# Performance work log

Measured on AMD Instinct MI355X. Metric: run time of the kernel, lower is better.

The kernel has to match this reference:

```python
import jax, jax.numpy as jnp
import numpy as np

EPS = 1e-12
TAU = 1.0

def _normalize(x, axis=-1):
    # matches torch.nn.functional.normalize (p=2, eps=1e-12)
    n = jnp.linalg.norm(x, axis=axis, keepdims=True)
    return x / jnp.maximum(n, EPS)

def setup_inputs() -> dict:
    key = jax.random.key(0)
    ks = jax.random.split(key, 6)
    N, B, D, K = 8192, 512, 64, 4
    input_rating = jax.random.uniform(ks[0], (B, N), dtype=jnp.float32)
    # row-normalized-scale adjacency (mimics a normalized item-item graph)
    item_adj = jax.random.uniform(ks[1], (N, N), dtype=jnp.float32) * (2.0 / N)
    item_emb = jax.random.normal(ks[2], (N, D), dtype=jnp.float32) * float(np.sqrt(2.0 / (N + D)))
    proto_emb = jax.random.normal(ks[3], (K, D), dtype=jnp.float32) * float(np.sqrt(2.0 / (K + D)))
    enc_w = jax.random.normal(ks[4], (2 * D, N), dtype=jnp.float32) * float(np.sqrt(2.0 / (N + 2 * D)))
    enc_b = jax.random.normal(ks[5], (2 * D,), dtype=jnp.float32) * 0.01
    return {"input_rating": input_rating, "item_adj": item_adj, "item_emb": item_emb,
            "proto_emb": proto_emb, "enc_w": enc_w, "enc_b": enc_b}

def reference(input_rating, item_adj, item_emb, proto_emb, enc_w, enc_b):
    D = enc_b.shape[0] // 2
    prototypes = _normalize(proto_emb)          # [K, D]
    items = _normalize(item_emb)                # [N, D]
    cates = jax.nn.softmax(items @ prototypes.T / TAU, axis=-1)  # [N, K] (eval: mode branch)
    # per-prototype masked ratings, vectorized over K: [K, B, N]
    x_k = input_rating[None, :, :] * cates.T[:, None, :]
    x_k = _normalize(x_k)                       # fn.normalize(x_k, p=2) over items dim
    # two-hop propagation through dense item-item adjacency
    tmp = jnp.einsum('kbn,nm->kbm', x_k, item_adj)
    tmp = jnp.einsum('kbn,nm->kbm', tmp, item_adj)
    x = (tmp + x_k) / 2.0                       # dropout is identity in eval
    h = jnp.einsum('kbn,on->kbo', x, enc_w) + enc_b  # [K, B, 2D]
    mu = _normalize(h[..., :D])                 # [K, B, D]
    logvar = -h[..., D:]                        # [K, B, D]
    z = _normalize(mu)                          # eval: reparameterize returns mu
    logits_k = jnp.einsum('kbd,nd->kbn', z, items) / TAU
    probs = jnp.sum(jnp.exp(logits_k) * cates.T[:, None, :], axis=0)  # [B, N]
    logits = jnp.log(probs)
    return logits, mu, logvar
```

## Files before the change

kernel.cpp:

```cpp
#include <hip/hip_runtime.h>

typedef __attribute__((ext_vector_type(8))) short short8;
typedef __attribute__((ext_vector_type(4))) float f32x4;

#define AS3P(x) ((__attribute__((address_space(3))) void*)(x))
#define AS1P(x) ((const __attribute__((address_space(1))) void*)(x))

__device__ __forceinline__ unsigned short f2bf(float f) {
    unsigned int u = __float_as_uint(f);
    u += 0x7fffu + ((u >> 16) & 1u);
    return (unsigned short)(u >> 16);
}
__device__ __forceinline__ float bf2f(unsigned short b) {
    return __uint_as_float(((unsigned int)b) << 16);
}
__device__ __forceinline__ unsigned int pk2bf(float a, float b) {
    return (unsigned int)f2bf(a) | ((unsigned int)f2bf(b) << 16);
}
__device__ __forceinline__ float waveReduceSum(float v) {
    #pragma unroll
    for (int off = 32; off; off >>= 1) v += __shfl_xor(v, off, 64);
    return v;
}

__global__ __launch_bounds__(256) void k_mega(const float* __restrict__ adj,
                                              unsigned short* __restrict__ adj_bf,
                                              const float* __restrict__ enc_w,
                                              unsigned short* __restrict__ encw,
                                              const float* __restrict__ item_emb,
                                              const float* __restrict__ proto,
                                              unsigned short* __restrict__ items_bf,
                                              float* __restrict__ catesT) {
    __shared__ float sp[256];
    int bx = blockIdx.x, tid = threadIdx.x;
    if (bx < 32768) {
        size_t i = ((size_t)bx * 256 + tid) * 8;
        f32x4 a = __builtin_nontemporal_load((const f32x4*)(adj + i));
        f32x4 b = __builtin_nontemporal_load((const f32x4*)(adj + i + 4));
        uint4 pk;
        pk.x = pk2bf(a[0], a[1]); pk.y = pk2bf(a[2], a[3]);
        pk.z = pk2bf(b[0], b[1]); pk.w = pk2bf(b[2], b[3]);
        *(uint4*)(adj_bf + i) = pk;
        return;
    }
    if (bx < 33280) {
        size_t i = (((size_t)bx - 32768) * 256 + tid) * 8;
        float4 a = *(const float4*)(enc_w + i);
        float4 b = *(const float4*)(enc_w + i + 4);
        uint4 pk;
        pk.x = pk2bf(a.x, a.y); pk.y = pk2bf(a.z, a.w);
        pk.z = pk2bf(b.x, b.y); pk.w = pk2bf(b.z, b.w);
        *(uint4*)(encw + i) = pk;
        return;
    }
    sp[tid] = proto[tid];
    __syncthreads();
    {
        float v = sp[tid];
        float ss = waveReduceSum(v * v);
        sp[tid] = v * (1.f / fmaxf(sqrtf(ss), 1e-12f));
    }
    __syncthreads();
    int i = (bx - 33280) * 256 + tid;
    const float4* row = (const float4*)(item_emb + (size_t)i * 64);
    float4 f[16];
    float ss = 0.f;
    #pragma unroll
    for (int q = 0; q < 16; ++q) {
        f[q] = row[q];
        ss += f[q].x * f[q].x + f[q].y * f[q].y + f[q].z * f[q].z + f[q].w * f[q].w;
    }
    float inv = 1.f / fmaxf(sqrtf(ss), 1e-12f);
    float dots[4] = {0.f, 0.f, 0.f, 0.f};
    unsigned short* ob = items_bf + (size_t)i * 64;
    #pragma unroll
    for (int q = 0; q < 16; ++q) {
        f[q].x *= inv; f[q].y *= inv; f[q].z *= inv; f[q].w *= inv;
        #pragma unroll
        for (int k = 0; k < 4; ++k) {
            dots[k] += f[q].x * sp[k * 64 + q * 4 + 0] + f[q].y * sp[k * 64 + q * 4 + 1]
                     + f[q].z * sp[k * 64 + q * 4 + 2] + f[q].w * sp[k * 64 + q * 4 + 3];
        }
    }
    #pragma unroll
    for (int q = 0; q < 16; q += 2) {
        uint4 pk;
        pk.x = pk2bf(f[q].x, f[q].y);         pk.y = pk2bf(f[q].z, f[q].w);
        pk.z = pk2bf(f[q + 1].x, f[q + 1].y); pk.w = pk2bf(f[q + 1].z, f[q + 1].w);
        *(uint4*)(ob + q * 4) = pk;
    }
    float m = fmaxf(fmaxf(dots[0], dots[1]), fmaxf(dots[2], dots[3]));
    float e0 = expf(dots[0] - m), e1 = expf(dots[1] - m), e2 = expf(dots[2] - m), e3 = expf(dots[3] - m);
    float is = 1.f / (e0 + e1 + e2 + e3);
    catesT[0 * 8192 + i] = e0 * is;
    catesT[1 * 8192 + i] = e1 * is;
    catesT[2 * 8192 + i] = e2 * is;
    catesT[3 * 8192 + i] = e3 * is;
}

__global__ __launch_bounds__(256) void k_gemm_part(const unsigned short* __restrict__ A,
                                                   const unsigned short* __restrict__ B,
                                                   unsigned short* __restrict__ Cout,
                                                   int M, int ksplit, int lda, int ldb, int ldc) {
    __shared__ unsigned short lA[128 * 64];
    __shared__ unsigned short lB[128 * 64];
    int tid = threadIdx.x;
    int lane = tid & 63;
    int w = tid >> 6;
    int wr = w >> 1, wc = w & 1;
    int mBase = blockIdx.y * 128;
    int nBase = blockIdx.x * 128;
    int Kbeg = blockIdx.z * ksplit;
    int Kend = Kbeg + ksplit;

    f32x4 acc[4][4] = {};

    const unsigned short* Ablk = A + (size_t)mBase * lda;
    const unsigned short* Bblk = B + (size_t)nBase * ldb;
    int srow = tid >> 3;
    int scg = (tid & 7) ^ (srow & 7);
    char* ldsA_w = (char*)lA + w * 1024;
    char* ldsB_w = (char*)lB + w * 1024;

    for (int k0 = Kbeg; k0 < Kend; k0 += 64) {
        __syncthreads();
        #pragma unroll
        for (int it = 0; it < 4; ++it) {
            const unsigned short* ga = Ablk + (size_t)(it * 32 + srow) * lda + k0 + scg * 8;
            __builtin_amdgcn_global_load_lds(AS1P(ga), AS3P(ldsA_w + it * 4096), 16, 0, 0);
            const unsigned short* gb = Bblk + (size_t)(it * 32 + srow) * ldb + k0 + scg * 8;
            __builtin_amdgcn_global_load_lds(AS1P(gb), AS3P(ldsB_w + it * 4096), 16, 0, 0);
        }
        __syncthreads();
        #pragma unroll
        for (int kk = 0; kk < 2; ++kk) {
            short8 af[4], bfr[4];
            #pragma unroll
            for (int i = 0; i < 4; ++i) {
                int rowa = wr * 64 + i * 16 + (lane & 15);
                int slot = kk * 4 + (lane >> 4);
                af[i] = *(const short8*)((const char*)lA + rowa * 128 + ((slot ^ (rowa & 7)) * 16));
                int rowb = wc * 64 + i * 16 + (lane & 15);
                bfr[i] = *(const short8*)((const char*)lB + rowb * 128 + ((slot ^ (rowb & 7)) * 16));
            }
            #pragma unroll
            for (int i = 0; i < 4; ++i)
                #pragma unroll
                for (int j = 0; j < 4; ++j)
                    acc[i][j] = __builtin_amdgcn_mfma_f32_16x16x32_bf16(af[i], bfr[j], acc[i][j], 0, 0, 0);
        }
    }

    unsigned short* outP = Cout + (size_t)blockIdx.z * M * ldc;
    #pragma unroll
    for (int i = 0; i < 4; ++i) {
        int rbase = mBase + wr * 64 + i * 16 + (lane >> 4) * 4;
        #pragma unroll
        for (int j = 0; j < 4; ++j) {
            int col = nBase + wc * 64 + j * 16 + (lane & 15);
            #pragma unroll
            for (int r = 0; r < 4; ++r)
                outP[(size_t)(rbase + r) * ldc + col] = f2bf(acc[i][j][r]);
        }
    }
}

__global__ __launch_bounds__(256) void k_redW(const unsigned short* __restrict__ part,
                                              unsigned short* __restrict__ W1T,
                                              const float* __restrict__ rating,
                                              const float* __restrict__ catesT,
                                              unsigned short* __restrict__ rating_bf,
                                              float* __restrict__ inv4) {
    int tid = threadIdx.x;
    if (blockIdx.x < 512) {
        size_t base = ((size_t)blockIdx.x * 256 + tid) * 8;
        float a[8] = {0.f,0.f,0.f,0.f,0.f,0.f,0.f,0.f};
        #pragma unroll
        for (int sp = 0; sp < 8; ++sp) {
            uint4 v = *(const uint4*)(part + (size_t)sp * 1048576 + base);
            a[0] += bf2f((unsigned short)(v.x & 0xffff)); a[1] += bf2f((unsigned short)(v.x >> 16));
            a[2] += bf2f((unsigned short)(v.y & 0xffff)); a[3] += bf2f((unsigned short)(v.y >> 16));
            a[4] += bf2f((unsigned short)(v.z & 0xffff)); a[5] += bf2f((unsigned short)(v.z >> 16));
            a[6] += bf2f((unsigned short)(v.w & 0xffff)); a[7] += bf2f((unsigned short)(v.w >> 16));
        }
        uint4 pk;
        pk.x = pk2bf(a[0], a[1]); pk.y = pk2bf(a[2], a[3]);
        pk.z = pk2bf(a[4], a[5]); pk.w = pk2bf(a[6], a[7]);
        *(uint4*)(W1T + base) = pk;
        return;
    }
    __shared__ float t[16];
    int b = blockIdx.x - 512;
    const float* row = rating + (size_t)b * 8192;
    float s0 = 0.f, s1 = 0.f, s2 = 0.f, s3 = 0.f;
    #pragma unroll
    for (int j = 0; j < 8; ++j) {
        int i4 = tid + j * 256;
        f32x4 r = __builtin_nontemporal_load((const f32x4*)(row + i4 * 4));
        ushort4 pk;
        pk.x = f2bf(r[0]); pk.y = f2bf(r[1]); pk.z = f2bf(r[2]); pk.w = f2bf(r[3]);
        *(ushort4*)(rating_bf + (size_t)b * 8192 + i4 * 4) = pk;
        float4 c0 = *(const float4*)(catesT + 0 * 8192 + i4 * 4);
        float4 c1 = *(const float4*)(catesT + 1 * 8192 + i4 * 4);
        float4 c2 = *(const float4*)(catesT + 2 * 8192 + i4 * 4);
        float4 c3 = *(const float4*)(catesT + 3 * 8192 + i4 * 4);
        float px, py, pz, pw;
        px = r[0] * c0.x; py = r[1] * c0.y; pz = r[2] * c0.z; pw = r[3] * c0.w;
        s0 += px * px + py * py + pz * pz + pw * pw;
        px = r[0] * c1.x; py = r[1] * c1.y; pz = r[2] * c1.z; pw = r[3] * c1.w;
        s1 += px * px + py * py + pz * pz + pw * pw;
        px = r[0] * c2.x; py = r[1] * c2.y; pz = r[2] * c2.z; pw = r[3] * c2.w;
        s2 += px * px + py * py + pz * pz + pw * pw;
        px = r[0] * c3.x; py = r[1] * c3.y; pz = r[2] * c3.z; pw = r[3] * c3.w;
        s3 += px * px + py * py + pz * pz + pw * pw;
    }
    s0 = waveReduceSum(s0); s1 = waveReduceSum(s1);
    s2 = waveReduceSum(s2); s3 = waveReduceSum(s3);
    if ((tid & 63) == 0) {
        int w = tid >> 6;
        t[w * 4 + 0] = s0; t[w * 4 + 1] = s1; t[w * 4 + 2] = s2; t[w * 4 + 3] = s3;
    }
    __syncthreads();
    if (tid < 4) {
        float ss = t[0 * 4 + tid] + t[1 * 4 + tid] + t[2 * 4 + tid] + t[3 * 4 + tid];
        inv4[b * 4 + tid] = 1.f / fmaxf(sqrtf(ss), 1e-12f);
    }
}

__global__ __launch_bounds__(256) void k_red_G(const unsigned short* __restrict__ part,
                                               const float* __restrict__ enc_w,
                                               const float* __restrict__ catesT,
                                               unsigned short* __restrict__ G) {
    size_t base = ((size_t)blockIdx.x * 256 + threadIdx.x) * 8;
    int o = (int)(base >> 13);
    int n = (int)(base & 8191);
    float a[8] = {0.f,0.f,0.f,0.f,0.f,0.f,0.f,0.f};
    #pragma unroll
    for (int sp = 0; sp < 8; ++sp) {
        uint4 v = *(const uint4*)(part + (size_t)sp * 1048576 + base);
        a[0] += bf2f((unsigned short)(v.x & 0xffff)); a[1] += bf2f((unsigned short)(v.x >> 16));
        a[2] += bf2f((unsigned short)(v.y & 0xffff)); a[3] += bf2f((unsigned short)(v.y >> 16));
        a[4] += bf2f((unsigned short)(v.z & 0xffff)); a[5] += bf2f((unsigned short)(v.z >> 16));
        a[6] += bf2f((unsigned short)(v.w & 0xffff)); a[7] += bf2f((unsigned short)(v.w >> 16));
    }
    float4 e0 = *(const float4*)(enc_w + base);
    float4 e1 = *(const float4*)(enc_w + base + 4);
    a[0] = 0.5f * (a[0] + e0.x); a[1] = 0.5f * (a[1] + e0.y);
    a[2] = 0.5f * (a[2] + e0.z); a[3] = 0.5f * (a[3] + e0.w);
    a[4] = 0.5f * (a[4] + e1.x); a[5] = 0.5f * (a[5] + e1.y);
    a[6] = 0.5f * (a[6] + e1.z); a[7] = 0.5f * (a[7] + e1.w);
    #pragma unroll
    for (int k = 0; k < 4; ++k) {
        float4 c0 = *(const float4*)(catesT + (size_t)k * 8192 + n);
        float4 c1 = *(const float4*)(catesT + (size_t)k * 8192 + n + 4);
        uint4 pk;
        pk.x = pk2bf(a[0] * c0.x, a[1] * c0.y); pk.y = pk2bf(a[2] * c0.z, a[3] * c0.w);
        pk.z = pk2bf(a[4] * c1.x, a[5] * c1.y); pk.w = pk2bf(a[6] * c1.z, a[7] * c1.w);
        *(uint4*)(G + (size_t)(k * 128 + o) * 8192 + n) = pk;
    }
}

__global__ __launch_bounds__(128) void k_reduce_h2(const unsigned short* __restrict__ hpart,
                                                   const float* __restrict__ enc_b,
                                                   const float* __restrict__ inv4,
                                                   unsigned short* __restrict__ mu_bf,
                                                   float* __restrict__ outp) {
    int r = blockIdx.x;
    int k = r >> 9, b = r & 511;
    int o = threadIdx.x;
    float s = 0.f;
    #pragma unroll
    for (int sp = 0; sp < 32; ++sp)
        s += bf2f(hpart[(size_t)sp * 262144 + (size_t)b * 512 + k * 128 + o]);
    s = s * inv4[b * 4 + k] + enc_b[o];
    const size_t MU0 = (size_t)512 * 8192;
    const size_t LV0 = MU0 + (size_t)2048 * 64;
    if (o < 64) {
        float ss = s * s;
        #pragma unroll
        for (int off = 32; off; off >>= 1) ss += __shfl_xor(ss, off, 64);
        float inv = 1.f / fmaxf(sqrtf(ss), 1e-12f);
        float mv = s * inv;
        outp[MU0 + (size_t)r * 64 + o] = mv;
        mu_bf[(size_t)r * 64 + o] = f2bf(mv);
    } else {
        outp[LV0 + (size_t)r * 64 + (o - 64)] = -s;
    }
}

__global__ __launch_bounds__(256) void k_logits_mfma(const unsigned short* __restrict__ mu_bf,
                                                     const unsigned short* __restrict__ items_bf,
                                                     const float* __restrict__ catesT,
                                                     float* __restrict__ out) {
    __shared__ unsigned short lA[128 * 64];
    __shared__ unsigned short lB[128 * 64];
    int tid = threadIdx.x;
    int lane = tid & 63, w = tid >> 6, wr = w >> 1, wc = w & 1;
    int nBase = blockIdx.x * 128, bBase = blockIdx.y * 128;
    int srow = tid >> 3;
    int scg = (tid & 7) ^ (srow & 7);
    char* ldsA_w = (char*)lA + w * 1024;
    char* ldsB_w = (char*)lB + w * 1024;

    #pragma unroll
    for (int it = 0; it < 4; ++it) {
        const unsigned short* gb = items_bf + (size_t)(nBase + it * 32 + srow) * 64 + scg * 8;
        __builtin_amdgcn_global_load_lds(AS1P(gb), AS3P(ldsB_w + it * 4096), 16, 0, 0);
    }

    f32x4 p[4][4] = {};
    for (int k = 0; k < 4; ++k) {
        __syncthreads();
        #pragma unroll
        for (int it = 0; it < 4; ++it) {
            const unsigned short* ga = mu_bf + (size_t)(k * 512 + bBase + it * 32 + srow) * 64 + scg * 8;
            __builtin_amdgcn_global_load_lds(AS1P(ga), AS3P(ldsA_w + it * 4096), 16, 0, 0);
        }
        __syncthreads();
        f32x4 acc[4][4] = {};
        #pragma unroll
        for (int kk = 0; kk < 2; ++kk) {
            short8 af[4], bfr[4];
            #pragma unroll
            for (int i = 0; i < 4; ++i) {
                int rowa = wr * 64 + i * 16 + (lane & 15);
                int slot = kk * 4 + (lane >> 4);
                af[i] = *(const short8*)((const char*)lA + rowa * 128 + ((slot ^ (rowa & 7)) * 16));
                int rowb = wc * 64 + i * 16 + (lane & 15);
                bfr[i] = *(const short8*)((const char*)lB + rowb * 128 + ((slot ^ (rowb & 7)) * 16));
            }
            #pragma unroll
            for (int i = 0; i < 4; ++i)
                #pragma unroll
                for (int j = 0; j < 4; ++j)
                    acc[i][j] = __builtin_amdgcn_mfma_f32_16x16x32_bf16(af[i], bfr[j], acc[i][j], 0, 0, 0);
        }
        #pragma unroll
        for (int j = 0; j < 4; ++j) {
            int col = nBase + wc * 64 + j * 16 + (lane & 15);
            float c = catesT[(size_t)k * 8192 + col];
            #pragma unroll
            for (int i = 0; i < 4; ++i)
                #pragma unroll
                for (int r = 0; r < 4; ++r)
                    p[i][j][r] += __expf(acc[i][j][r]) * c;
        }
    }
    #pragma unroll
    for (int i = 0; i < 4; ++i) {
        int rbase = bBase + wr * 64 + i * 16 + (lane >> 4) * 4;
        #pragma unroll
        for (int j = 0; j < 4; ++j) {
            int col = nBase + wc * 64 + j * 16 + (lane & 15);
            #pragma unroll
            for (int r = 0; r < 4; ++r)
                out[(size_t)(rbase + r) * 8192 + col] = __logf(p[i][j][r]);
        }
    }
}

extern "C" void kernel_launch(void* const* d_in, const int* in_sizes, int n_in,
                              void* d_out, int out_size, void* d_ws, size_t ws_size,
                              hipStream_t stream) {
    const float* rating   = (const float*)d_in[0];
    const float* adj      = (const float*)d_in[1];
    const float* item_emb = (const float*)d_in[2];
    const float* proto    = (const float*)d_in[3];
    const float* enc_w    = (const float*)d_in[4];
    const float* enc_b    = (const float*)d_in[5];
    float* out = (float*)d_out;

    char* ws = (char*)d_ws;
    unsigned short* adj_bf    = (unsigned short*)ws;
    unsigned short* part_bf   = adj_bf + (size_t)8192 * 8192;
    unsigned short* rating_bf = part_bf + (size_t)8 * 1048576;
    unsigned short* G         = rating_bf + (size_t)512 * 8192;
    unsigned short* W1T       = G + (size_t)512 * 8192;
    unsigned short* encw      = W1T + (size_t)128 * 8192;
    unsigned short* hpart     = encw + (size_t)128 * 8192;
    unsigned short* items_bf  = hpart + (size_t)32 * 262144;
    unsigned short* mu_bf     = items_bf + (size_t)8192 * 64;
    float* catesT = (float*)(mu_bf + (size_t)2048 * 64);
    float* inv4   = catesT + (size_t)4 * 8192;

    k_mega<<<33312, 256, 0, stream>>>(adj, adj_bf, enc_w, encw, item_emb, proto, items_bf, catesT);

    k_gemm_part<<<dim3(64, 1, 8), 256, 0, stream>>>(encw, adj_bf, part_bf, 128, 1024, 8192, 8192, 8192);
    k_redW<<<1024, 256, 0, stream>>>(part_bf, W1T, rating, catesT, rating_bf, inv4);

    k_gemm_part<<<dim3(64, 1, 8), 256, 0, stream>>>(W1T, adj_bf, part_bf, 128, 1024, 8192, 8192, 8192);
    k_red_G<<<512, 256, 0, stream>>>(part_bf, enc_w, catesT, G);

    k_gemm_part<<<dim3(4, 4, 32), 256, 0, stream>>>(rating_bf, G, hpart, 512, 256, 8192, 8192, 512);
    k_reduce_h2<<<2048, 128, 0, stream>>>(hpart, enc_b, inv4, mu_bf, out);

    k_logits_mfma<<<dim3(64, 4), 256, 0, stream>>>(mu_bf, items_bf, catesT, out);
}
```

Measured before the change: 179.7 us.

## Double-buffer LDS tiles in split-K GEMM to overlap loads with MFMA

The GEMM kernel now uses two LDS buffers for the A and B tiles. It issues the global-to-LDS loads for the next K-step before computing on the current one, so only one barrier per iteration remains. The aim is to hide global memory latency behind the MFMA work. In exchange, LDS use per block doubles to 64 KB, which can lower occupancy.

```diff
diff --git a/kernel.cpp b/kernel.cpp
--- a/kernel.cpp
+++ b/kernel.cpp
@@ -102,8 +102,8 @@
                                                    const unsigned short* __restrict__ B,
                                                    unsigned short* __restrict__ Cout,
                                                    int M, int ksplit, int lda, int ldb, int ldc) {
-    __shared__ unsigned short lA[128 * 64];
-    __shared__ unsigned short lB[128 * 64];
+    __shared__ unsigned short lA[2][128 * 64];
+    __shared__ unsigned short lB[2][128 * 64];
     int tid = threadIdx.x;
     int lane = tid & 63;
     int w = tid >> 6;
@@ -119,19 +119,25 @@
     const unsigned short* Bblk = B + (size_t)nBase * ldb;
     int srow = tid >> 3;
     int scg = (tid & 7) ^ (srow & 7);
-    char* ldsA_w = (char*)lA + w * 1024;
-    char* ldsB_w = (char*)lB + w * 1024;
-
+
+    #define STAGE(buf, k0)                                                                     \
+        do {                                                                                   \
+            char* ldsA_w = (char*)lA[buf] + w * 1024;                                          \
+            char* ldsB_w = (char*)lB[buf] + w * 1024;                                          \
+            _Pragma("unroll")                                                                  \
+            for (int it = 0; it < 4; ++it) {                                                   \
+                const unsigned short* ga = Ablk + (size_t)(it * 32 + srow) * lda + (k0) + scg * 8; \
+                __builtin_amdgcn_global_load_lds(AS1P(ga), AS3P(ldsA_w + it * 4096), 16, 0, 0);    \
+                const unsigned short* gb = Bblk + (size_t)(it * 32 + srow) * ldb + (k0) + scg * 8; \
+                __builtin_amdgcn_global_load_lds(AS1P(gb), AS3P(ldsB_w + it * 4096), 16, 0, 0);    \
+            }                                                                                  \
+        } while (0)
+
+    STAGE(0, Kbeg);
+    __syncthreads();
+    int cur = 0;
     for (int k0 = Kbeg; k0 < Kend; k0 += 64) {
-        __syncthreads();
-        #pragma unroll
-        for (int it = 0; it < 4; ++it) {
-            const unsigned short* ga = Ablk + (size_t)(it * 32 + srow) * lda + k0 + scg * 8;
-            __builtin_amdgcn_global_load_lds(AS1P(ga), AS3P(ldsA_w + it * 4096), 16, 0, 0);
-            const unsigned short* gb = Bblk + (size_t)(it * 32 + srow) * ldb + k0 + scg * 8;
-            __builtin_amdgcn_global_load_lds(AS1P(gb), AS3P(ldsB_w + it * 4096), 16, 0, 0);
-        }
-        __syncthreads();
+        if (k0 + 64 < Kend) STAGE(cur ^ 1, k0 + 64);
         #pragma unroll
         for (int kk = 0; kk < 2; ++kk) {
             short8 af[4], bfr[4];
@@ -139,9 +145,9 @@
             for (int i = 0; i < 4; ++i) {
                 int rowa = wr * 64 + i * 16 + (lane & 15);
                 int slot = kk * 4 + (lane >> 4);
-                af[i] = *(const short8*)((const char*)lA + rowa * 128 + ((slot ^ (rowa & 7)) * 16));
+                af[i] = *(const short8*)((const char*)lA[cur] + rowa * 128 + ((slot ^ (rowa & 7)) * 16));
                 int rowb = wc * 64 + i * 16 + (lane & 15);
-                bfr[i] = *(const short8*)((const char*)lB + rowb * 128 + ((slot ^ (rowb & 7)) * 16));
+                bfr[i] = *(const short8*)((const char*)lB[cur] + rowb * 128 + ((slot ^ (rowb & 7)) * 16));
             }
             #pragma unroll
             for (int i = 0; i < 4; ++i)
@@ -149,7 +155,10 @@
                 for (int j = 0; j < 4; ++j)
                     acc[i][j] = __builtin_amdgcn_mfma_f32_16x16x32_bf16(af[i], bfr[j], acc[i][j], 0, 0, 0);
         }
-    }
+        __syncthreads();
+        cur ^= 1;
+    }
+    #undef STAGE
 
     unsigned short* outP = Cout + (size_t)blockIdx.z * M * ldc;
     #pragma unroll
```

Result: faster. 175.0 us (-2.6%).
